# Performance work log

Measured on AMD Instinct MI355X. Metric: run time of the kernel, lower is better.

## Reference

```python
import jax, jax.numpy as jnp
import numpy as np

BS, P, D, C, ND, K, NC, H = 32, 196, 512, 100, 51, 50, 800, 8
LAMBDA, BETA, EPS = 0.5, 5.5, 1e-5


def _ln(x, g, b):
    m = x.mean(-1, keepdims=True)
    v = jnp.mean((x - m) ** 2, axis=-1, keepdims=True)
    return (x - m) / jnp.sqrt(v + EPS) * g + b


def _norm(x):
    return x / jnp.linalg.norm(x, axis=-1, keepdims=True)


def _bonder(x, kv, Wq, Wk, Wv, Wo, ln1_g, ln1_b, ln2_g, ln2_b, W1, b1, W2, b2):
    # cross-attn block: queries = text prompts [B,N,d], kv = retrieved patch feats [B,M,d]
    B, N, d = x.shape
    M = kv.shape[1]
    dh = d // H
    q = (_ln(x, ln1_g, ln1_b) @ Wq).reshape(B, N, H, dh)
    k = (kv @ Wk).reshape(B, M, H, dh)
    v = (kv @ Wv).reshape(B, M, H, dh)
    att = jax.nn.softmax(jnp.einsum('bnhd,bmhd->bhnm', q, k) / np.sqrt(dh).astype(np.float32), axis=-1)
    o = jnp.einsum('bhnm,bmhd->bnhd', att, v).reshape(B, N, d) @ Wo
    x = x + o
    h = _ln(x, ln2_g, ln2_b)
    return x + jax.nn.gelu(h @ W1 + b1) @ W2 + b2


def _dense_logits(gfeat, local, all_text, mean_text, topk):
    # gfeat [b,d], local [b,p,d], all_text [C,n,d], mean_text [C,d]
    base = gfeat @ mean_text.T                                   # [b,C]
    w = jnp.einsum('bd,bpd->bp', gfeat, local)                   # [b,p]
    atf = jnp.transpose(all_text, (1, 0, 2))                     # [n,C,d]
    v = jax.nn.softmax(jnp.einsum('cd,ncd->nc', mean_text, atf), axis=0)  # [n,C]
    sim = jnp.einsum('bpd,ncd->bcpn', local, atf)                # [b,C,p,n]
    vals, idx = jax.lax.top_k(jnp.transpose(sim, (0, 1, 3, 2)), topk)     # over patch dim
    sim_topk = jnp.transpose(vals, (0, 1, 3, 2))                 # [b,C,k,n]
    idx = jnp.transpose(idx, (0, 1, 3, 2))                       # [b,C,k,n]
    idx_w = idx[:, 0, :, 0]                                      # [b,k]
    w_topk = jax.nn.softmax(jnp.take_along_axis(w, idx_w, axis=1), axis=-1)  # [b,k]
    weight = jnp.einsum('bk,nc->bckn', w_topk, v)                # [b,C,k,n]
    return base + jnp.sum(sim_topk * weight, axis=(-2, -1))


def setup_inputs() -> dict:
    key = jax.random.key(0)
    ks = jax.random.split(key, 12)
    s = 0.02
    labels = jax.random.randint(ks[10], (BS,), 0, C)
    cache_labels = jax.random.randint(ks[11], (NC,), 0, C)
    return {
        'local_feat': jax.random.normal(ks[0], (BS, P, D)),
        'Wa': jnp.eye(D) + s * jax.random.normal(ks[1], (D, D)),
        'text_cache': jax.random.normal(ks[2], (C, ND, D)),
        'Wq': s * jax.random.normal(ks[3], (D, D)),
        'Wk': s * jax.random.normal(ks[4], (D, D)),
        'Wv': s * jax.random.normal(ks[5], (D, D)),
        'Wo': s * jax.random.normal(ks[6], (D, D)),
        'ln1_g': jnp.ones((D,)), 'ln1_b': jnp.zeros((D,)),
        'ln2_g': jnp.ones((D,)), 'ln2_b': jnp.zeros((D,)),
        'W1': s * jax.random.normal(ks[7], (D, 4 * D)), 'b1': jnp.zeros((4 * D,)),
        'W2': s * jax.random.normal(ks[8], (4 * D, D)), 'b2': jnp.zeros((D,)),
        'logit_scale': jnp.asarray(np.log(1.0 / 0.07), jnp.float32),
        'ensemble_scale': jnp.asarray(-2.0, jnp.float32),
        'raw_cache_local_feats': jax.random.normal(ks[9], (NC, P, D)),
        'cache_values': jax.nn.one_hot(cache_labels, C, dtype=jnp.float32),
        'labels': labels,
        'cache_labels': cache_labels,
    }


def reference(local_feat, Wa, text_cache, Wq, Wk, Wv, Wo, ln1_g, ln1_b, ln2_g, ln2_b,
              W1, b1, W2, b2, logit_scale, ensemble_scale, raw_cache_local_feats,
              cache_values, labels, cache_labels):
    bs = local_feat.shape[0]
    adapted_local = _norm(local_feat @ Wa.T)                      # [b,p,d]
    adapted_global = _norm(adapted_local.mean(axis=1))            # [b,d]
    base_text_mean = _norm(jax.lax.stop_gradient(text_cache).mean(axis=1))  # [C,d]
    sim_to_text = jax.lax.stop_gradient(adapted_local @ base_text_mean.T)   # [b,p,C]
    sim_target = sim_to_text[jnp.arange(bs), :, labels]           # [b,p]
    topk_idx = jax.lax.top_k(sim_target, K)[1]
    botk_idx = jax.lax.top_k(-sim_target, K)[1]
    topk_feats = jnp.take_along_axis(adapted_local, topk_idx[:, :, None], axis=1)  # [b,K,d]
    botk_feats = jnp.take_along_axis(adapted_local, botk_idx[:, :, None], axis=1)
    # training branch: bonder on ground-truth class prompts, scatter into bias_full
    l2p = text_cache[labels]                                      # [b,ND,d]
    text_bias = _bonder(l2p, jax.lax.stop_gradient(topk_feats),
                        Wq, Wk, Wv, Wo, ln1_g, ln1_b, ln2_g, ln2_b, W1, b1, W2, b2)
    bias_full = jnp.zeros((bs, C, ND, D), local_feat.dtype).at[jnp.arange(bs), labels].set(text_bias)
    bias_avg = bias_full.mean(axis=0)                             # [C,ND,d]
    refined = text_cache + LAMBDA * bias_avg
    refined_norm = _norm(refined)
    refined_mean_norm = _norm(refined_norm.mean(axis=1))
    ls = jnp.exp(logit_scale)
    inter = ls * _dense_logits(adapted_global, adapted_local, refined_norm, refined_mean_norm, K)
    # tip-adapter cache branch
    cache_adapted = _norm(raw_cache_local_feats @ Wa.T)           # [Nc,p,d]
    cache_sim = jax.lax.stop_gradient(cache_adapted @ base_text_mean.T)
    cache_sim_target = cache_sim[jnp.arange(cache_sim.shape[0]), :, cache_labels]
    cache_topk_idx = jax.lax.top_k(cache_sim_target, K)[1]
    cache_topk_feats = jnp.take_along_axis(cache_adapted, cache_topk_idx[:, :, None], axis=1)
    cache_keys = _norm(cache_topk_feats.mean(axis=1))             # [Nc,d]
    query_keys = _norm(topk_feats.mean(axis=1))                   # [b,d]
    affinity = jnp.exp(-BETA * (1.0 - query_keys @ cache_keys.T))
    intra = affinity @ cache_values                               # [b,C]
    scale = jax.nn.sigmoid(ensemble_scale)
    logits = inter * (1 - scale) + intra * ls * scale
    return (logits, inter, intra, adapted_global, topk_feats, botk_feats, refined_norm)
```

## Files before the change

### kernel.cpp

```cpp
#include <hip/hip_runtime.h>
#include <math.h>

#define DEV static __device__ __forceinline__

typedef __attribute__((ext_vector_type(8))) short short8v;
typedef __attribute__((ext_vector_type(8))) _Float16 half8v;
typedef __attribute__((ext_vector_type(4))) float f32x4;

DEV unsigned encf(float f){ unsigned b=__float_as_uint(f); return b ^ (0x80000000u | (unsigned)((int)b>>31)); }
DEV unsigned long long pkvi(float v, int idx){
  return ((unsigned long long)encf(v)<<32) | (unsigned long long)(0xffffffffu - (unsigned)idx);
}
DEV unsigned long long wave_max_ull(unsigned long long u){
  #pragma unroll
  for (int m=1;m<64;m<<=1){ unsigned long long o = __shfl_xor(u, m); if (o>u) u=o; }
  return u;
}
DEV float wave_sum(float v){
  #pragma unroll
  for (int m=32;m;m>>=1) v += __shfl_xor(v, m);
  return v;
}
DEV float blk_sum256(float v, float* scr){
  v = wave_sum(v);
  __syncthreads();
  if ((threadIdx.x & 63)==0) scr[threadIdx.x>>6] = v;
  __syncthreads();
  return scr[0]+scr[1]+scr[2]+scr[3];
}
DEV float gelu_f(float x){ return 0.5f*x*(1.f + tanhf(0.7978845608028654f*(x + 0.044715f*x*x*x))); }
DEV unsigned short f2bf(float x){
  unsigned u = __float_as_uint(x);
  unsigned r = (u + 0x7fffu + ((u>>16)&1u)) >> 16;
  return (unsigned short)r;
}
DEV float bf2f(unsigned short h){ return __uint_as_float(((unsigned)h)<<16); }
DEV void gld16(const void* g, void* l){
  __builtin_amdgcn_global_load_lds((const __attribute__((address_space(1))) unsigned int*)g,
                                   (__attribute__((address_space(3))) unsigned int*)l, 16, 0, 0);
}
template<int CTRL>
DEV float dppf(float x){
  return __int_as_float(__builtin_amdgcn_mov_dpp(__float_as_int(x), CTRL, 0xF, 0xF, false));
}

template<bool TRANSB, int EPI>
__global__ __launch_bounds__(256,2) void gemm128(
  const float* __restrict__ A, const float* __restrict__ B, float* __restrict__ Cp,
  const int M, const int N, const int K,
  const float* __restrict__ bias, const float* __restrict__ resid)
{
  __shared__ float As[16][132];
  __shared__ float Bs[16][132];
  const int t = threadIdx.x;
  const int row0 = blockIdx.x*128, col0 = blockIdx.y*128;
  const int tx = t & 15, ty = t >> 4;
  float acc[8][8];
  #pragma unroll
  for (int i=0;i<8;++i)
    #pragma unroll
    for (int j=0;j<8;++j) acc[i][j]=0.f;

  for (int k0=0; k0<K; k0+=16){
    #pragma unroll
    for (int it=0; it<2; ++it){
      int f = t + it*256;
      int m = f >> 2, kq = (f & 3) << 2;
      float4 v = make_float4(0.f,0.f,0.f,0.f);
      int gr = row0 + m;
      if (gr < M) v = *(const float4*)(A + (size_t)gr*K + (k0+kq));
      As[kq+0][m]=v.x; As[kq+1][m]=v.y; As[kq+2][m]=v.z; As[kq+3][m]=v.w;
    }
    if (TRANSB){
      #pragma unroll
      for (int it=0; it<2; ++it){
        int f = t + it*256;
        int n = f >> 2, kq = (f & 3) << 2;
        float4 v = make_float4(0.f,0.f,0.f,0.f);
        int gc = col0 + n;
        if (gc < N) v = *(const float4*)(B + (size_t)gc*K + (k0+kq));
        Bs[kq+0][n]=v.x; Bs[kq+1][n]=v.y; Bs[kq+2][n]=v.z; Bs[kq+3][n]=v.w;
      }
    } else {
      #pragma unroll
      for (int it=0; it<2; ++it){
        int f = t + it*256;
        int kk = f >> 5, n4 = (f & 31) << 2;
        float4 v = *(const float4*)(B + (size_t)(k0+kk)*N + (col0+n4));
        *(float4*)&Bs[kk][n4] = v;
      }
    }
    __syncthreads();
    #pragma unroll
    for (int k=0;k<16;++k){
      float a[8], bb[8];
      *(float4*)&a[0] = *(const float4*)&As[k][ty*4];
      *(float4*)&a[4] = *(const float4*)&As[k][64+ty*4];
      *(float4*)&bb[0] = *(const float4*)&Bs[k][tx*4];
      *(float4*)&bb[4] = *(const float4*)&Bs[k][64+tx*4];
      #pragma unroll
      for (int i=0;i<8;++i)
        #pragma unroll
        for (int j=0;j<8;++j) acc[i][j] = fmaf(a[i], bb[j], acc[i][j]);
    }
    __syncthreads();
  }

  #pragma unroll
  for (int i=0;i<8;++i){
    int gr = row0 + ((i<4)? (ty*4+i) : (64+ty*4+i-4));
    if (gr >= M) continue;
    #pragma unroll
    for (int jb=0;jb<2;++jb){
      int gc = col0 + (jb? (64+tx*4) : (tx*4));
      float4 vv;
      vv.x = acc[i][jb*4+0]; vv.y = acc[i][jb*4+1]; vv.z = acc[i][jb*4+2]; vv.w = acc[i][jb*4+3];
      if (EPI & 1){
        const float4 bv = *(const float4*)(bias + gc);
        vv.x += bv.x; vv.y += bv.y; vv.z += bv.z; vv.w += bv.w;
      }
      if (EPI & 2){
        vv.x = gelu_f(vv.x); vv.y = gelu_f(vv.y); vv.z = gelu_f(vv.z); vv.w = gelu_f(vv.w);
      }
      if (EPI & 4){
        const float4 rv = *(const float4*)(resid + (size_t)gr*N + gc);
        vv.x += rv.x; vv.y += rv.y; vv.z += rv.z; vv.w += rv.w;
      }
      *(float4*)(Cp + (size_t)gr*N + gc) = vv;
    }
  }
}

template<bool TRANS, bool SUBI>
__global__ __launch_bounds__(256) void k_convw(const float* __restrict__ W,
    unsigned short* __restrict__ hi, unsigned short* __restrict__ lo, int R, int C){
  int n = blockIdx.x;
  int K = TRANS ? R : C;
  for (int k = threadIdx.x; k < K; k += 256){
    float x = TRANS ? W[(size_t)k*C + n] : W[(size_t)n*C + k];
    if (SUBI && k==n) x -= 1.f;
    unsigned short h = f2bf(x);
    hi[(size_t)n*K + k] = h;
    if (lo) lo[(size_t)n*K + k] = f2bf(x - bf2f(h));
  }
}

__global__ __launch_bounds__(256) void k_convw4(
  const float* __restrict__ Wq, const float* __restrict__ Wk,
  const float* __restrict__ Wv, const float* __restrict__ Wo,
  unsigned short* __restrict__ qh, unsigned short* __restrict__ ql,
  unsigned short* __restrict__ kh, unsigned short* __restrict__ kl,
  unsigned short* __restrict__ vh, unsigned short* __restrict__ vl,
  unsigned short* __restrict__ oh, unsigned short* __restrict__ ol)
{
  int n = blockIdx.x;
  const float* W; unsigned short *hi, *lo;
  switch(blockIdx.y){
    case 0: W=Wq; hi=qh; lo=ql; break;
    case 1: W=Wk; hi=kh; lo=kl; break;
    case 2: W=Wv; hi=vh; lo=vl; break;
    default: W=Wo; hi=oh; lo=ol; break;
  }
  for (int k = threadIdx.x; k < 512; k += 256){
    float x = W[(size_t)k*512 + n];
    unsigned short h = f2bf(x);
    hi[(size_t)n*512 + k] = h;
    lo[(size_t)n*512 + k] = f2bf(x - bf2f(h));
  }
}

__global__ __launch_bounds__(256) void k_convd2(const float* __restrict__ Wa, unsigned short* __restrict__ Dfrag){
  int e = blockIdx.x;
  int tile = e>>4, lr = e&15;
  for (int d = threadIdx.x; d < 512; d += 256){
    float x = Wa[(size_t)e*512 + d] - (e==d ? 1.f : 0.f);
    union { _Float16 hh; unsigned short u; } cv;
    cv.hh = (_Float16)x;
    int ks = d>>5, q = (d>>3)&3, el = d&7;
    Dfrag[(size_t)(((tile*16+ks)*64 + q*16 + lr)*8 + el)] = cv.u;
  }
}

template<int EPI>
__global__ __launch_bounds__(256,2) void gemmMF(
  const float* __restrict__ A, const unsigned short* __restrict__ Bhi,
  const unsigned short* __restrict__ Blo, float* __restrict__ Cp,
  const int M, const int N, const int K,
  const float* __restrict__ bias, const float* __restrict__ resid)
{
  __shared__ __align__(16) char sm[32768];
  const int t = threadIdx.x, lane = t&63, wid = t>>6;
  const int row0 = blockIdx.x*128, col0 = blockIdx.y*128;
  f32x4 acc[2][8];
  #pragma unroll
  for (int i=0;i<2;++i)
    #pragma unroll
    for (int j=0;j<8;++j) acc[i][j] = (f32x4){0.f,0.f,0.f,0.f};

  int offA[2], offB[8];
  #pragma unroll
  for (int mt=0; mt<2; ++mt){
    int row = (2*wid+mt)*16 + (lane&15);
    int sp = (lane>>4) ^ ((row>>1)&3);
    offA[mt] = row*64 + sp*16;
  }
  #pragma unroll
  for (int nt=0; nt<8; ++nt){
    int row = nt*16 + (lane&15);
    int sp = (lane>>4) ^ ((row>>1)&3);
    offB[nt] = row*64 + sp*16;
  }

  const int nks = K >> 5;
  for (int ks=0; ks<nks; ++ks){
    #pragma unroll
    for (int i=0;i<2;++i){
      int s = i*256 + t, row = s>>2, sl2 = s&3, phys = sl2 ^ ((row>>1)&3);
      int gr = row0 + row;
      float4 p0 = make_float4(0.f,0.f,0.f,0.f), p1 = p0;
      if (gr < M){
        const float* gp = A + (size_t)gr*K + ks*32 + sl2*8;
        p0 = *(const float4*)gp; p1 = *(const float4*)(gp+4);
      }
      float xs[8] = {p0.x,p0.y,p0.z,p0.w,p1.x,p1.y,p1.z,p1.w};
      union { unsigned short u[8]; float4 f; } uh, ul;
      #pragma unroll
      for (int u=0;u<8;++u){
        unsigned short h = f2bf(xs[u]);
        uh.u[u] = h;
        ul.u[u] = f2bf(xs[u] - bf2f(h));
      }
      *(float4*)(sm + row*64 + phys*16) = uh.f;
      *(float4*)(sm + 8192 + row*64 + phys*16) = ul.f;
    }
    #pragma unroll
    for (int i=0;i<2;++i){
      int s = i*256 + t, row = s>>2, sl2 = s&3, slog = sl2 ^ ((row>>1)&3);
      size_t goff = (size_t)(col0+row)*K + ks*32 + slog*8;
      gld16(Bhi + goff, sm + 16384 + (i*256 + wid*64)*16);
      gld16(Blo + goff, sm + 24576 + (i*256 + wid*64)*16);
    }
    __syncthreads();
    short8v ah0 = *(short8v*)(sm + offA[0]);
    short8v ah1 = *(short8v*)(sm + offA[1]);
    short8v al0 = *(short8v*)(sm + 8192 + offA[0]);
    short8v al1 = *(short8v*)(sm + 8192 + offA[1]);
    #pragma unroll
    for (int nt=0; nt<8; ++nt){
      short8v bh = *(short8v*)(sm + 16384 + offB[nt]);
      short8v bl = *(short8v*)(sm + 24576 + offB[nt]);
      acc[0][nt] = __builtin_amdgcn_mfma_f32_16x16x32_bf16(ah0, bh, acc[0][nt], 0,0,0);
      acc[0][nt] = __builtin_amdgcn_mfma_f32_16x16x32_bf16(ah0, bl, acc[0][nt], 0,0,0);
      acc[0][nt] = __builtin_amdgcn_mfma_f32_16x16x32_bf16(al0, bh, acc[0][nt], 0,0,0);
      acc[1][nt] = __builtin_amdgcn_mfma_f32_16x16x32_bf16(ah1, bh, acc[1][nt], 0,0,0);
      acc[1][nt] = __builtin_amdgcn_mfma_f32_16x16x32_bf16(ah1, bl, acc[1][nt], 0,0,0);
      acc[1][nt] = __builtin_amdgcn_mfma_f32_16x16x32_bf16(al1, bh, acc[1][nt], 0,0,0);
    }
    __syncthreads();
  }

  #pragma unroll
  for (int mt=0; mt<2; ++mt){
    #pragma unroll
    for (int nt=0; nt<8; ++nt){
      int n = col0 + nt*16 + (lane&15);
      int mb = row0 + (2*wid+mt)*16 + (lane>>4)*4;
      #pragma unroll
      for (int j=0;j<4;++j){
        int m = mb + j;
        if (m < M){
          float v = acc[mt][nt][j];
          if (EPI & 1) v += bias[n];
          if (EPI & 2) v = gelu_f(v);
          if (EPI & 4) v += resid[(size_t)m*N + n];
          Cp[(size_t)m*N + n] = v;
        }
      }
    }
  }
}

__global__ __launch_bounds__(512,1) void k_un7(
  const float* __restrict__ raw, const unsigned short* __restrict__ Dfrag,
  const float* __restrict__ zm, const int* __restrict__ clab,
  float* __restrict__ cdot, float* __restrict__ norm2)
{
  __shared__ __align__(16) char Alds[131072];
  __shared__ float n2sq[128];
  __shared__ float n2x[4][128];
  const int t = threadIdx.x, lane = t&63;
  const int wid = t>>6, wm = wid>>2, wn = wid&3;
  const int m0 = blockIdx.x*128;

  {
    const int row = t>>2, sl = t&3;
    const int slg = sl ^ ((row>>1)&3);
    const float* rp = raw + ((size_t)(m0+row))*512 + slg*8;
    const float* zp = zm + (size_t)clab[(m0+row)/196]*512 + slg*8;
    float sq=0.f, cd=0.f;
    for (int ks=0; ks<16; ++ks){
      float4 p0 = *(const float4*)(rp + ks*32);
      float4 p1 = *(const float4*)(rp + ks*32 + 4);
      float4 z0 = *(const float4*)(zp + ks*32);
      float4 z1 = *(const float4*)(zp + ks*32 + 4);
      float xs[8] = {p0.x,p0.y,p0.z,p0.w,p1.x,p1.y,p1.z,p1.w};
      float zs[8] = {z0.x,z0.y,z0.z,z0.w,z1.x,z1.y,z1.z,z1.w};
      union { _Float16 h[8]; f32x4 f; } uh;
      #pragma unroll
      for (int u=0;u<8;++u){
        uh.h[u] = (_Float16)xs[u];
        sq = fmaf(xs[u],xs[u],sq);
        cd = fmaf(xs[u],zs[u],cd);
      }
      *(f32x4*)(Alds + ks*8192 + t*16) = uh.f;
    }
    sq += __shfl_xor(sq,1); sq += __shfl_xor(sq,2);
    cd += __shfl_xor(cd,1); cd += __shfl_xor(cd,2);
    if (sl==0){ n2sq[row] = sq; cdot[m0+row] = cd; }
  }
  __syncthreads();

  int offA[4];
  #pragma unroll
  for (int mt=0; mt<4; ++mt){
    int row = wm*64 + mt*16 + (lane&15);
    int sp = (lane>>4) ^ ((row>>1)&3);
    offA[mt] = row*64 + sp*16;
  }
  const half8v* Dv = (const half8v*)Dfrag;

  float pacc[4][4];
  #pragma unroll
  for (int a_=0;a_<4;++a_)
    #pragma unroll
    for (int b_=0;b_<4;++b_) pacc[a_][b_]=0.f;

  for (int eb2=0; eb2<4; ++eb2){
    f32x4 acc[4][2];
    #pragma unroll
    for (int a_=0;a_<4;++a_)
      #pragma unroll
      for (int b_=0;b_<2;++b_) acc[a_][b_] = (f32x4){0.f,0.f,0.f,0.f};

    #pragma unroll 4
    for (int ks=0; ks<16; ++ks){
      half8v af[4], bf[2];
      #pragma unroll
      for (int mt=0; mt<4; ++mt) af[mt] = *(half8v*)(Alds + ks*8192 + offA[mt]);
      #pragma unroll
      for (int nt=0; nt<2; ++nt) bf[nt] = Dv[(size_t)(((eb2*8 + wn*2 + nt)*16 + ks)*64 + lane)];
      #pragma unroll
      for (int mt=0; mt<4; ++mt)
        #pragma unroll
        for (int nt=0; nt<2; ++nt)
          acc[mt][nt] = __builtin_amdgcn_mfma_f32_16x16x32_f16(af[mt], bf[nt], acc[mt][nt], 0,0,0);
    }

    #pragma unroll
    for (int mt=0; mt<4; ++mt){
      #pragma unroll
      for (int j=0;j<4;++j){
        int row = wm*64 + mt*16 + (lane>>4)*4 + j;
        float p = 0.f;
        #pragma unroll
        for (int nt=0; nt<2; ++nt){
          float U = acc[mt][nt][j];
          int eg = eb2*128 + wn*32 + nt*16 + (lane&15);
          int kse = eg>>5, o = eg&31;
          int sll = (o>>3) ^ ((row>>1)&3);
          float rh = (float)*(const _Float16*)(Alds + kse*8192 + row*64 + sll*16 + (o&7)*2);
          p = fmaf(U, 2.f*rh + U, p);
        }
        p += __shfl_xor(p,1); p += __shfl_xor(p,2); p += __shfl_xor(p,4); p += __shfl_xor(p,8);
        pacc[mt][j] += p;
      }
    }
  }

  __syncthreads();
  if ((lane&15)==0){
    #pragma unroll
    for (int mt=0; mt<4; ++mt)
      #pragma unroll
      for (int j=0;j<4;++j)
        n2x[wn][wm*64 + mt*16 + (lane>>4)*4 + j] = pacc[mt][j];
  }
  __syncthreads();
  if (t < 128)
    norm2[m0+t] = n2sq[t] + n2x[0][t] + n2x[1][t] + n2x[2][t] + n2x[3][t];
}

__global__ __launch_bounds__(256) void k_rownorm(const float* __restrict__ in, float* __restrict__ out,
                                                 unsigned short* __restrict__ bfo, int nrows){
  __shared__ float scr[4];
  int r = blockIdx.x, t = threadIdx.x; (void)nrows;
  const float* p = in + (size_t)r*512;
  float x0 = p[t], x1 = p[t+256];
  float ss = blk_sum256(x0*x0 + x1*x1, scr);
  float inv = 1.f/sqrtf(ss);
  float v0 = x0*inv, v1 = x1*inv;
  out[(size_t)r*512 + t] = v0;
  out[(size_t)r*512 + t + 256] = v1;
  if (bfo){
    size_t br = (size_t)(r/196)*256 + (r%196);
    bfo[br*512 + t]     = f2bf(v0);
    bfo[br*512 + t+256] = f2bf(v1);
  }
}

__global__ __launch_bounds__(256) void k_meanrows_norm(const float* __restrict__ in, int nper,
                                                       float* __restrict__ o1, float* __restrict__ o2){
  __shared__ float scr[4];
  int g = blockIdx.x, t = threadIdx.x;
  float s0=0.f, s1=0.f;
  const float* bp = in + (size_t)g*nper*512;
  for (int r=0;r<nper;++r){ s0 += bp[(size_t)r*512+t]; s1 += bp[(size_t)r*512+t+256]; }
  float ss = blk_sum256(s0*s0+s1*s1, scr);
  float inv = 1.f/sqrtf(ss);
  float v0 = s0*inv, v1 = s1*inv;
  o1[(size_t)g*512+t]=v0; o1[(size_t)g*512+t+256]=v1;
  if (o2){ o2[(size_t)g*512+t]=v0; o2[(size_t)g*512+t+256]=v1; }
}

__global__ __launch_bounds__(256) void k_zmat(const float* __restrict__ btm, const float* __restrict__ Wa, float* __restrict__ z){
  int c = blockIdx.x, t = threadIdx.x;
  float a0=0.f, a1=0.f;
  for (int d=0; d<512; ++d){
    float bv = btm[c*512+d];
    a0 = fmaf(bv, Wa[(size_t)d*512+t], a0);
    a1 = fmaf(bv, Wa[(size_t)d*512+t+256], a1);
  }
  z[c*512+t]=a0; z[c*512+t+256]=a1;
}

__global__ __launch_bounds__(256) void k_dot_bp(const float* __restrict__ AL, const float* __restrict__ vecs,
                                                const int* __restrict__ sel, float* __restrict__ outv, int mode){
  int wid = blockIdx.x*4 + (threadIdx.x>>6);
  int lane = threadIdx.x & 63;
  int b = wid/196;
  int vrow = sel ? sel[b] : (mode ? 0 : b);
  const float* a = AL + (size_t)wid*512 + lane*8;
  const float* v = vecs + (size_t)vrow*512 + lane*8;
  float4 a0 = *(const float4*)a, a1 = *(const float4*)(a+4);
  float4 v0 = *(const float4*)v, v1 = *(const float4*)(v+4);
  float s = a0.x*v0.x + a0.y*v0.y + a0.z*v0.z + a0.w*v0.w
          + a1.x*v1.x + a1.y*v1.y + a1.z*v1.z + a1.w*v1.w;
  s = wave_sum(s);
  if (lane==0) outv[wid] = s;
}

__global__ __launch_bounds__(256) void k_dot2(const float* __restrict__ AL, const float* __restrict__ AGw,
                                              const float* __restrict__ RN00,
                                              float* __restrict__ wbp, float* __restrict__ sLw){
  int wid = blockIdx.x*4 + (threadIdx.x>>6);
  int lane = threadIdx.x & 63;
  int b = wid/196;
  const float* a = AL + (size_t)wid*512 + lane*8;
  const float* v = AGw + (size_t)b*512 + lane*8;
  const float* w = RN00 + lane*8;
  float4 a0=*(const float4*)a, a1=*(const float4*)(a+4);
  float4 v0=*(const float4*)v, v1=*(const float4*)(v+4);
  float4 w0=*(const float4*)w, w1=*(const float4*)(w+4);
  float s1 = a0.x*v0.x+a0.y*v0.y+a0.z*v0.z+a0.w*v0.w + a1.x*v1.x+a1.y*v1.y+a1.z*v1.z+a1.w*v1.w;
  float s2 = a0.x*w0.x+a0.y*w0.y+a0.z*w0.z+a0.w*w0.w + a1.x*w1.x+a1.y*w1.y+a1.z*w1.z+a1.w*w1.w;
  s1 = wave_sum(s1); s2 = wave_sum(s2);
  if (lane==0){ wbp[wid] = s1; sLw[wid] = s2; }
}

__global__ __launch_bounds__(64) void k_topbot(const float* __restrict__ st, int* __restrict__ tki, int* __restrict__ bki){
  int b = blockIdx.x, lane = threadIdx.x;
  float v[4];
  #pragma unroll
  for (int s2=0;s2<4;++s2){ int p = lane + 64*s2; v[s2] = (p<196)? st[b*196+p] : -INFINITY; }
  for (int k=0;k<50;++k){
    unsigned long long best = pkvi(v[0], lane);
    { unsigned long long cc=pkvi(v[1],lane+64);  if(cc>best)best=cc; }
    { unsigned long long cc=pkvi(v[2],lane+128); if(cc>best)best=cc; }
    { unsigned long long cc=pkvi(v[3],lane+192); if(cc>best)best=cc; }
    best = wave_max_ull(best);
    int widx = (int)(0xffffffffu - (unsigned)(best & 0xffffffffu));
    if (lane==0) tki[b*50+k] = widx;
    if ((widx & 63)==lane) v[widx>>6] = -INFINITY;
  }
  #pragma unroll
  for (int s2=0;s2<4;++s2){ int p = lane + 64*s2; v[s2] = (p<196)? -st[b*196+p] : -INFINITY; }
  for (int k=0;k<50;++k){
    unsigned long long best = pkvi(v[0], lane);
    { unsigned long long cc=pkvi(v[1],lane+64);  if(cc>best)best=cc; }
    { unsigned long long cc=pkvi(v[2],lane+128); if(cc>best)best=cc; }
    { unsigned long long cc=pkvi(v[3],lane+192); if(cc>best)best=cc; }
    best = wave_max_ull(best);
    int widx = (int)(0xffffffffu - (unsigned)(best & 0xffffffffu));
    if (lane==0) bki[b*50+k] = widx;
    if ((widx & 63)==lane) v[widx>>6] = -INFINITY;
  }
}

__global__ __launch_bounds__(256) void k_gather_tb(const float* __restrict__ AL, const int* __restrict__ tki, const int* __restrict__ bki,
                                                   float* __restrict__ otk, float* __restrict__ obk, float* __restrict__ qk){
  __shared__ float scr[4];
  int b = blockIdx.x, t = threadIdx.x;
  float a0=0.f, a1=0.f;
  for (int k=0;k<50;++k){
    int pt = tki[b*50+k];
    const float* rp = AL + ((size_t)b*196+pt)*512;
    float x0 = rp[t], x1 = rp[t+256];
    otk[((size_t)b*50+k)*512 + t] = x0; otk[((size_t)b*50+k)*512 + t+256] = x1;
    a0 += x0; a1 += x1;
    int pb = bki[b*50+k];
    const float* rb = AL + ((size_t)b*196+pb)*512;
    obk[((size_t)b*50+k)*512 + t] = rb[t]; obk[((size_t)b*50+k)*512 + t+256] = rb[t+256];
  }
  float ss = blk_sum256(a0*a0+a1*a1, scr);
  float inv = 1.f/sqrtf(ss);
  qk[b*512+t] = a0*inv; qk[b*512+t+256] = a1*inv;
}

__global__ __launch_bounds__(256) void k_gather_x(const float* __restrict__ tc, const int* __restrict__ labels, float* __restrict__ xb){
  int r = blockIdx.x, t = threadIdx.x;
  int b = r/51, n = r%51;
  int lab = labels[b];
  const float* src = tc + ((size_t)lab*51 + n)*512;
  xb[(size_t)r*512+t] = src[t]; xb[(size_t)r*512+t+256] = src[t+256];
}

__global__ __launch_bounds__(256) void k_layernorm(const float* __restrict__ in, float* __restrict__ out,
                                                   const float* __restrict__ g, const float* __restrict__ be){
  __shared__ float scr[4];
  int r = blockIdx.x, t = threadIdx.x;
  const float* p = in + (size_t)r*512;
  float x0=p[t], x1=p[t+256];
  float s = blk_sum256(x0+x1, scr);
  float mean = s*(1.f/512.f);
  float ss = blk_sum256(x0*x0+x1*x1, scr);
  float var = ss*(1.f/512.f) - mean*mean;
  float inv = 1.f/sqrtf(var + 1e-5f);
  out[(size_t)r*512+t]     = (x0-mean)*inv*g[t]     + be[t];
  out[(size_t)r*512+t+256] = (x1-mean)*inv*g[t+256] + be[t+256];
}

__global__ __launch_bounds__(256) void k_attn(const float* __restrict__ qb, const float* __restrict__ kb,
                                              const float* __restrict__ vb, float* __restrict__ ob){
  int b = blockIdx.x, h = blockIdx.y, t = threadIdx.x;
  __shared__ float qh[51][65];
  __shared__ float kh[50][65];
  __shared__ float vh[50][65];
  __shared__ float S[51][52];
  for (int f=t; f<51*64; f+=256){ int n=f>>6, d=f&63; qh[n][d] = qb[((size_t)(b*51+n))*512 + h*64 + d]; }
  for (int f=t; f<50*64; f+=256){ int m=f>>6, d=f&63;
    kh[m][d] = kb[((size_t)(b*50+m))*512 + h*64 + d];
    vh[m][d] = vb[((size_t)(b*50+m))*512 + h*64 + d];
  }
  __syncthreads();
  for (int f=t; f<51*50; f+=256){
    int n=f/50, m=f%50;
    float s=0.f;
    #pragma unroll 8
    for (int d=0; d<64; ++d) s = fmaf(qh[n][d], kh[m][d], s);
    S[n][m] = s*0.125f;
  }
  __syncthreads();
  int w = t>>6, lane = t&63;
  for (int n=w; n<51; n+=4){
    float x = (lane<50)? S[n][lane] : -INFINITY;
    float mx = x;
    #pragma unroll
    for (int m2=32;m2;m2>>=1) mx = fmaxf(mx, __shfl_xor(mx,m2));
    float e = (lane<50)? expf(x-mx) : 0.f;
    float se = wave_sum(e);
    if (lane<50) S[n][lane] = e/se;
  }
  __syncthreads();
  for (int f=t; f<51*64; f+=256){
    int n=f>>6, d=f&63;
    float s=0.f;
    #pragma unroll 10
    for (int m=0;m<50;++m) s = fmaf(S[n][m], vh[m][d], s);
    ob[((size_t)(b*51+n))*512 + h*64 + d] = s;
  }
}

__global__ __launch_bounds__(256) void k_refined(const float* __restrict__ tc, const float* __restrict__ TB,
                                                 const int* __restrict__ labels, float* __restrict__ RN,
                                                 unsigned short* __restrict__ RNbf){
  __shared__ float scr[4];
  __shared__ int labL[32];
  int blk = blockIdx.x, t = threadIdx.x;
  int c = blk/51, n = blk%51;
  if (t<32) labL[t] = labels[t];
  __syncthreads();
  float r0=0.f, r1=0.f;
  for (int b=0;b<32;++b){
    if (labL[b]==c){
      const float* tb = TB + ((size_t)(b*51+n))*512;
      r0 += tb[t]; r1 += tb[t+256];
    }
  }
  const float* tcp = tc + ((size_t)(c*51+n))*512;
  r0 = tcp[t]     + r0*(1.f/64.f);
  r1 = tcp[t+256] + r1*(1.f/64.f);
  float ss = blk_sum256(r0*r0+r1*r1, scr);
  float inv = 1.f/sqrtf(ss);
  float v0 = r0*inv, v1 = r1*inv;
  RN[((size_t)(c*51+n))*512+t]     = v0;
  RN[((size_t)(c*51+n))*512+t+256] = v1;
  size_t br = (size_t)c*64 + n;
  RNbf[br*512 + t]     = f2bf(v0);
  RNbf[br*512 + t+256] = f2bf(v1);
}

__global__ __launch_bounds__(256) void k_vsm(const float* __restrict__ RN, const float* __restrict__ RMN, float* __restrict__ vsm){
  __shared__ float sv[51];
  int c = blockIdx.x, t = threadIdx.x, w = t>>6, lane = t&63;
  for (int n=w; n<51; n+=4){
    const float* a = RN + ((size_t)(c*51+n))*512 + lane*8;
    const float* m = RMN + (size_t)c*512 + lane*8;
    float4 a0=*(const float4*)a, a1=*(const float4*)(a+4);
    float4 m0=*(const float4*)m, m1=*(const float4*)(m+4);
    float s = a0.x*m0.x+a0.y*m0.y+a0.z*m0.z+a0.w*m0.w + a1.x*m1.x+a1.y*m1.y+a1.z*m1.z+a1.w*m1.w;
    s = wave_sum(s);
    if (lane==0) sv[n]=s;
  }
  __syncthreads();
  if (t<64){
    float x = (t<51)? sv[t] : -INFINITY;
    float mx = x;
    #pragma unroll
    for (int m2=32;m2;m2>>=1) mx = fmaxf(mx, __shfl_xor(mx,m2));
    float e = (t<51)? expf(x-mx) : 0.f;
    float se = wave_sum(e);
    if (t<51) vsm[c*51+t] = e/se;
  }
}

__global__ __launch_bounds__(64) void k_wtopk(const float* __restrict__ sLg,
                                              const float* __restrict__ wbp, float* __restrict__ wtk){
  __shared__ int idxL[50];
  int b = blockIdx.x, lane = threadIdx.x;
  float v[4];
  #pragma unroll
  for (int s2=0;s2<4;++s2){ int p = lane+64*s2; v[s2] = (p<196)? sLg[b*196+p] : -INFINITY; }
  for (int k=0;k<50;++k){
    unsigned long long best = pkvi(v[0], lane);
    { unsigned long long cc=pkvi(v[1],lane+64);  if(cc>best)best=cc; }
    { unsigned long long cc=pkvi(v[2],lane+128); if(cc>best)best=cc; }
    { unsigned long long cc=pkvi(v[3],lane+192); if(cc>best)best=cc; }
    best = wave_max_ull(best);
    int widx = (int)(0xffffffffu - (unsigned)(best & 0xffffffffu));
    if (lane==0) idxL[k]=widx;
    if ((widx&63)==lane) v[widx>>6] = -INFINITY;
  }
  __syncthreads();
  float wv = (lane<50)? wbp[b*196 + idxL[lane]] : -INFINITY;
  float mx = wv;
  #pragma unroll
  for (int m2=32;m2;m2>>=1) mx = fmaxf(mx, __shfl_xor(mx,m2));
  float e = (lane<50)? expf(wv-mx) : 0.f;
  float se = wave_sum(e);
  if (lane<50) wtk[b*50+lane] = e/se;
}

__global__ __launch_bounds__(256,3) void k_dense3(
  const unsigned short* __restrict__ ALbf, const unsigned short* __restrict__ RNbf,
  const float* __restrict__ RMN, const float* __restrict__ AG,
  const float* __restrict__ vsm, const float* __restrict__ wtk,
  const float* __restrict__ lsp, float* __restrict__ interw)
{
  __shared__ __align__(16) char smem[52224];
  __shared__ float red[8];
  __shared__ float wtkS[52];
  const int c = blockIdx.x, b = blockIdx.y;
  const int t = threadIdx.x, lane = t&63, wid = t>>6;

  if (t<50) wtkS[t] = wtk[b*50+t];
  if (t<64){
    const float* a = AG + (size_t)b*512 + t*8;
    const float* m = RMN + (size_t)c*512 + t*8;
    float4 a0=*(const float4*)a, a1=*(const float4*)(a+4);
    float4 m0=*(const float4*)m, m1=*(const float4*)(m+4);
    float s = a0.x*m0.x+a0.y*m0.y+a0.z*m0.z+a0.w*m0.w + a1.x*m1.x+a1.y*m1.y+a1.z*m1.z+a1.w*m1.w;
    s = wave_sum(s);
    if (t==0) red[4] = s;
  }

  f32x4 acc[4][4];
  #pragma unroll
  for (int i=0;i<4;++i)
    #pragma unroll
    for (int j=0;j<4;++j) acc[i][j] = (f32x4){0.f,0.f,0.f,0.f};

  int offA[4], offB[4];
  #pragma unroll
  for (int mt=0; mt<4; ++mt){
    int row = wid*64 + mt*16 + (lane&15);
    int sp = (lane>>4) ^ ((row>>1)&3);
    offA[mt] = row*64 + sp*16;
  }
  #pragma unroll
  for (int nt=0; nt<4; ++nt){
    int row = nt*16 + (lane&15);
    int sp = (lane>>4) ^ ((row>>1)&3);
    offB[nt] = row*64 + sp*16;
  }

  const unsigned short* Abase = ALbf + ((size_t)b<<17);
  const unsigned short* Bbase = RNbf + ((size_t)c<<15);

  auto STAGE = [&](int buf, int ks){
    const int Ab = buf? 20480 : 0, Bb = buf? 36864 : 16384;
    #pragma unroll
    for (int i=0;i<4;++i){
      int q = i*256 + t;
      int row = q>>2, sl = q&3;
      int slog = sl ^ ((row>>1)&3);
      gld16(Abase + ((size_t)row<<9) + ks*32 + slog*8, smem + Ab + (i*256 + wid*64)*16);
    }
    {
      int row = t>>2, sl = t&3;
      int slog = sl ^ ((row>>1)&3);
      gld16(Bbase + ((size_t)row<<9) + ks*32 + slog*8, smem + Bb + (wid*64)*16);
    }
  };

  STAGE(0, 0);
  __syncthreads();
  for (int ks=0; ks<16; ++ks){
    const int cur = ks&1;
    if (ks<15) STAGE(cur^1, ks+1);
    const int Ab = cur? 20480 : 0, Bb = cur? 36864 : 16384;
    short8v af[4], bf[4];
    #pragma unroll
    for (int mt=0; mt<4; ++mt) af[mt] = *(short8v*)(smem + Ab + offA[mt]);
    #pragma unroll
    for (int nt=0; nt<4; ++nt) bf[nt] = *(short8v*)(smem + Bb + offB[nt]);
    #pragma unroll
    for (int mt=0; mt<4; ++mt)
      #pragma unroll
      for (int nt=0; nt<4; ++nt)
        acc[mt][nt] = __builtin_amdgcn_mfma_f32_16x16x32_bf16(af[mt], bf[nt], acc[mt][nt], 0,0,0);
    __syncthreads();
  }

  #pragma unroll
  for (int mt=0; mt<4; ++mt){
    #pragma unroll
    for (int nt=0; nt<4; ++nt){
      int n = nt*16 + (lane&15);
      if (n < 51){
        int p0 = wid*64 + mt*16 + (lane>>4)*4;
        int addr = ((n<<10) + (p0<<2)) ^ ((((n&7)^wid)&7)<<4);
        *(f32x4*)(smem + addr) = acc[mt][nt];
      }
    }
  }
  __syncthreads();

  const int n = wid*16 + (lane>>2);
  const int q = lane&3;
  float v[64];
  if (n < 51){
    #pragma unroll
    for (int i=0;i<16;++i){
      int p = q*64 + i*4;
      int addr = ((n<<10) + (p<<2)) ^ ((((n&7)^q)&7)<<4);
      *(f32x4*)&v[i*4] = *(f32x4*)(smem + addr);
    }
  } else {
    #pragma unroll
    for (int i=0;i<64;++i) v[i] = -INFINITY;
  }
  if (q==3){
    #pragma unroll
    for (int j=4;j<64;++j) v[j] = -INFINITY;
  }

  #pragma unroll
  for (int k=2;k<=64;k<<=1){
    #pragma unroll
    for (int j=k>>1;j>=1;j>>=1){
      #pragma unroll
      for (int i=0;i<64;++i){
        if ((i&j)==0){
          int p2 = i|j;
          float a=v[i], bb=v[p2];
          if ((i&k)!=0){ v[i]=fminf(a,bb); v[p2]=fmaxf(a,bb); }
          else         { v[i]=fmaxf(a,bb); v[p2]=fminf(a,bb); }
        }
      }
    }
  }
  #pragma unroll
  for (int i=0;i<32;++i){
    float pa = dppf<0xB1>(v[63-i]);
    float pb = dppf<0xB1>(v[i]);
    v[i]    = fmaxf(v[i], pa);
    v[63-i] = fmaxf(v[63-i], pb);
  }
  #pragma unroll
  for (int j=32;j>=1;j>>=1){
    #pragma unroll
    for (int i=0;i<64;++i){
      if ((i&j)==0){ int p2=i|j; float a=v[i],bb=v[p2]; v[i]=fmaxf(a,bb); v[p2]=fminf(a,bb); }
    }
  }
  #pragma unroll
  for (int i=0;i<32;++i){
    float pa = dppf<0x4E>(v[63-i]);
    float pb = dppf<0x4E>(v[i]);
    v[i]    = fmaxf(v[i], pa);
    v[63-i] = fmaxf(v[63-i], pb);
  }
  #pragma unroll
  for (int j=32;j>=1;j>>=1){
    #pragma unroll
    for (int i=0;i<64;++i){
      if ((i&j)==0){ int p2=i|j; float a=v[i],bb=v[p2]; v[i]=fmaxf(a,bb); v[p2]=fminf(a,bb); }
    }
  }

  float s = 0.f;
  #pragma unroll
  for (int r=0;r<50;++r) s = fmaf(wtkS[r], v[r], s);
  float val = (q==0 && n<51) ? vsm[c*51+n]*s : 0.f;
  val = wave_sum(val);
  if (lane==0) red[wid] = val;
  __syncthreads();
  if (t==0){
    float ls = expf(lsp[0]);
    interw[b*100+c] = ls*(red[4] + red[0]+red[1]+red[2]+red[3]);
  }
}

__global__ __launch_bounds__(256) void k_cache_sel(const float* __restrict__ cdot, const float* __restrict__ norm2,
                                                   const float* __restrict__ raw, float* __restrict__ rbar){
  __shared__ int idxL[50];
  __shared__ float invL[50];
  int i = blockIdx.x, t = threadIdx.x;
  if (t < 64){
    int lane = t;
    float v[4];
    #pragma unroll
    for (int s2=0;s2<4;++s2){
      int p = lane+64*s2;
      v[s2] = (p<196)? cdot[(size_t)i*196+p] * (1.f/sqrtf(norm2[(size_t)i*196+p])) : -INFINITY;
    }
    for (int k=0;k<50;++k){
      unsigned long long best = pkvi(v[0], lane);
      { unsigned long long cc=pkvi(v[1],lane+64);  if(cc>best)best=cc; }
      { unsigned long long cc=pkvi(v[2],lane+128); if(cc>best)best=cc; }
      { unsigned long long cc=pkvi(v[3],lane+192); if(cc>best)best=cc; }
      best = wave_max_ull(best);
      int widx = (int)(0xffffffffu - (unsigned)(best & 0xffffffffu));
      if (lane==0){ idxL[k]=widx; invL[k] = 1.f/sqrtf(norm2[(size_t)i*196+widx]); }
      if ((widx&63)==lane) v[widx>>6] = -INFINITY;
    }
  }
  __syncthreads();
  float a0=0.f, a1=0.f;
  for (int k=0;k<50;++k){
    int p = idxL[k]; float iv = invL[k];
    const float* rp = raw + ((size_t)i*196+p)*512;
    a0 = fmaf(rp[t], iv, a0);
    a1 = fmaf(rp[t+256], iv, a1);
  }
  rbar[(size_t)i*512+t]=a0; rbar[(size_t)i*512+t+256]=a1;
}

__global__ __launch_bounds__(256) void k_aff(const float* __restrict__ qk, const float* __restrict__ ck, float* __restrict__ aff){
  int gid = blockIdx.x*4 + (threadIdx.x>>6);
  int lane = threadIdx.x&63;
  int b = gid/800, i = gid%800;
  const float* a = qk + (size_t)b*512 + lane*8;
  const float* v = ck + (size_t)i*512 + lane*8;
  float4 a0=*(const float4*)a, a1=*(const float4*)(a+4);
  float4 v0=*(const float4*)v, v1=*(const float4*)(v+4);
  float s = a0.x*v0.x+a0.y*v0.y+a0.z*v0.z+a0.w*v0.w + a1.x*v1.x+a1.y*v1.y+a1.z*v1.z+a1.w*v1.w;
  s = wave_sum(s);
  if (lane==0) aff[gid] = expf(-5.5f*(1.f - s));
}

__global__ __launch_bounds__(128) void k_intra(const float* __restrict__ aff, const float* __restrict__ cv, float* __restrict__ intra){
  __shared__ float affL[800];
  int b = blockIdx.x, t = threadIdx.x;
  for (int f=t; f<800; f+=128) affL[f] = aff[b*800+f];
  __syncthreads();
  if (t<100){
    float s=0.f;
    for (int i=0;i<800;++i) s = fmaf(affL[i], cv[(size_t)i*100+t], s);
    intra[b*100+t]=s;
  }
}

__global__ void k_final(const float* __restrict__ interw, const float* __restrict__ intraw,
                        const float* __restrict__ lsp, const float* __restrict__ esp, float* __restrict__ outp){
  int idx = blockIdx.x*256 + threadIdx.x;
  if (idx < 3200){
    float ls = expf(lsp[0]);
    float sc = 1.f/(1.f + expf(-esp[0]));
    float iv = interw[idx], ia = intraw[idx];
    outp[idx]        = iv*(1.f-sc) + ia*ls*sc;
    outp[3200+idx]   = iv;
    outp[6400+idx]   = ia;
  }
}

extern "C" void kernel_launch(void* const* d_in, const int* in_sizes, int n_in,
                              void* d_out, int out_size, void* d_ws, size_t ws_size,
                              hipStream_t stream)
{
  (void)in_sizes; (void)n_in; (void)out_size; (void)ws_size;
  const float* lf   = (const float*)d_in[0];
  const float* Wa   = (const float*)d_in[1];
  const float* tc   = (const float*)d_in[2];
  const float* Wq   = (const float*)d_in[3];
  const float* Wk   = (const float*)d_in[4];
  const float* Wv   = (const float*)d_in[5];
  const float* Wo   = (const float*)d_in[6];
  const float* ln1g = (const float*)d_in[7];
  const float* ln1b = (const float*)d_in[8];
  const float* ln2g = (const float*)d_in[9];
  const float* ln2b = (const float*)d_in[10];
  const float* W1   = (const float*)d_in[11];
  const float* b1   = (const float*)d_in[12];
  const float* W2   = (const float*)d_in[13];
  const float* b2   = (const float*)d_in[14];
  const float* lsp  = (const float*)d_in[15];
  const float* esp  = (const float*)d_in[16];
  const float* raw  = (const float*)d_in[17];
  const float* cv   = (const float*)d_in[18];
  const int* labels = (const int*)d_in[19];
  const int* clab   = (const int*)d_in[20];

  float* out = (float*)d_out;
  float* outAG = out + 9600;
  float* outTK = out + 25984;
  float* outBK = out + 845184;
  float* outRN = out + 1664384;

  float* wsf = (float*)d_ws;
  size_t o = 0;
  #define WALLOC(name, n) float* name = wsf + o; o += (size_t)(n);
  WALLOC(AL,    6272*512)
  WALLOC(xb,    1632*512)
  WALLOC(ln1x,  1632*512)
  WALLOC(qb,    1632*512)
  WALLOC(kb,    1600*512)
  WALLOC(vbuf,  1600*512)
  WALLOC(ob,    1632*512)
  WALLOC(x2,    1632*512)
  WALLOC(h2,    1632*512)
  WALLOC(y1g,   (size_t)1632*2048)
  WALLOC(TB,    1632*512)
  WALLOC(btm,   100*512)
  WALLOC(zm,    100*512)
  WALLOC(RMN,   100*512)
  WALLOC(vsm,   5100)
  WALLOC(st,    6272)
  WALLOC(wbp,   6272)
  WALLOC(sLw,   6272)
  WALLOC(AGw,   32*512)
  WALLOC(qkb,   32*512)
  WALLOC(wtk,   1600)
  WALLOC(norm2, 156800)
  WALLOC(cdot,  156800)
  WALLOC(rbar,  800*512)
  WALLOC(mbuf,  800*512)
  WALLOC(ckb,   800*512)
  WALLOC(aff,   25600)
  WALLOC(interw,3200)
  WALLOC(intraw,3200)
  #undef WALLOC
  int* tki = (int*)(wsf + o); o += 1600;
  int* bki = (int*)(wsf + o); o += 1600;
  unsigned short* ALbf = (unsigned short*)(wsf + o); o += (size_t)32*256*512/2;
  unsigned short* RNbf = (unsigned short*)(wsf + o); o += (size_t)100*64*512/2;
  #define WALLOC16(name, n) unsigned short* name = (unsigned short*)(wsf + o); o += ((size_t)(n))/2;
  WALLOC16(waHi, 262144)  WALLOC16(waLo, 262144)
  WALLOC16(wqHi, 262144)  WALLOC16(wqLo, 262144)
  WALLOC16(wkHi, 262144)  WALLOC16(wkLo, 262144)
  WALLOC16(wvHi, 262144)  WALLOC16(wvLo, 262144)
  WALLOC16(woHi, 262144)  WALLOC16(woLo, 262144)
  WALLOC16(w1Hi, 1048576) WALLOC16(w1Lo, 1048576)
  WALLOC16(w2Hi, 1048576) WALLOC16(w2Lo, 1048576)
  WALLOC16(dfrag, 262144)
  #undef WALLOC16

  k_convw<false,false><<<dim3(512), dim3(256), 0, stream>>>(Wa, waHi, waLo, 512,512);
  k_convw4<<<dim3(512,4), dim3(256), 0, stream>>>(Wq,Wk,Wv,Wo, wqHi,wqLo, wkHi,wkLo, wvHi,wvLo, woHi,woLo);
  k_convw<true ,false><<<dim3(2048), dim3(256), 0, stream>>>(W1, w1Hi, w1Lo, 512,2048);
  k_convw<true ,false><<<dim3(512), dim3(256), 0, stream>>>(W2, w2Hi, w2Lo, 2048,512);
  k_convd2<<<dim3(512), dim3(256), 0, stream>>>(Wa, dfrag);

  hipMemsetAsync(ALbf, 0, (size_t)32*256*512*2, stream);
  hipMemsetAsync(RNbf, 0, (size_t)100*64*512*2, stream);

  gemm128<true,0><<<dim3(49,4), dim3(256), 0, stream>>>(lf, Wa, AL, 6272,512,512, nullptr,nullptr);
  k_rownorm<<<dim3(6272), dim3(256), 0, stream>>>(AL, AL, ALbf, 6272);
  k_meanrows_norm<<<dim3(32), dim3(256), 0, stream>>>(AL, 196, AGw, outAG);
  k_meanrows_norm<<<dim3(100), dim3(256), 0, stream>>>(tc, 51, btm, (float*)nullptr);
  k_zmat<<<dim3(100), dim3(256), 0, stream>>>(btm, Wa, zm);
  k_dot_bp<<<dim3(1568), dim3(256), 0, stream>>>(AL, btm, labels, st, 0);
  k_topbot<<<dim3(32), dim3(64), 0, stream>>>(st, tki, bki);
  k_gather_tb<<<dim3(32), dim3(256), 0, stream>>>(AL, tki, bki, outTK, outBK, qkb);
  k_gather_x<<<dim3(1632), dim3(256), 0, stream>>>(tc, labels, xb);
  k_layernorm<<<dim3(1632), dim3(256), 0, stream>>>(xb, ln1x, ln1g, ln1b);
  gemmMF<0><<<dim3(13,4), dim3(256), 0, stream>>>(ln1x, wqHi, wqLo, qb, 1632,512,512, nullptr,nullptr);
  gemmMF<0><<<dim3(13,4), dim3(256), 0, stream>>>(outTK, wkHi, wkLo, kb, 1600,512,512, nullptr,nullptr);
  gemmMF<0><<<dim3(13,4), dim3(256), 0, stream>>>(outTK, wvHi, wvLo, vbuf, 1600,512,512, nullptr,nullptr);
  k_attn<<<dim3(32,8), dim3(256), 0, stream>>>(qb, kb, vbuf, ob);
  gemmMF<4><<<dim3(13,4), dim3(256), 0, stream>>>(ob, woHi, woLo, x2, 1632,512,512, nullptr, xb);
  k_layernorm<<<dim3(1632), dim3(256), 0, stream>>>(x2, h2, ln2g, ln2b);
  gemmMF<3><<<dim3(13,16), dim3(256), 0, stream>>>(h2, w1Hi, w1Lo, y1g, 1632,2048,512, b1, nullptr);
  gemmMF<5><<<dim3(13,4), dim3(256), 0, stream>>>(y1g, w2Hi, w2Lo, TB, 1632,512,2048, b2, x2);
  k_refined<<<dim3(5100), dim3(256), 0, stream>>>(tc, TB, labels, outRN, RNbf);
  k_meanrows_norm<<<dim3(100), dim3(256), 0, stream>>>(outRN, 51, RMN, (float*)nullptr);
  k_vsm<<<dim3(100), dim3(256), 0, stream>>>(outRN, RMN, vsm);
  k_dot2<<<dim3(1568), dim3(256), 0, stream>>>(AL, AGw, outRN, wbp, sLw);
  k_wtopk<<<dim3(32), dim3(64), 0, stream>>>(sLw, wbp, wtk);
  k_dense3<<<dim3(100,32), dim3(256), 0, stream>>>(ALbf, RNbf, RMN, AGw, vsm, wtk, lsp, interw);
  k_un7<<<dim3(1225), dim3(512), 0, stream>>>(raw, dfrag, zm, clab, cdot, norm2);
  k_cache_sel<<<dim3(800), dim3(256), 0, stream>>>(cdot, norm2, raw, rbar);
  gemmMF<0><<<dim3(7,4), dim3(256), 0, stream>>>(rbar, waHi, waLo, mbuf, 800,512,512, nullptr,nullptr);
  k_rownorm<<<dim3(800), dim3(256), 0, stream>>>(mbuf, ckb, (unsigned short*)nullptr, 800);
  k_aff<<<dim3(6400), dim3(256), 0, stream>>>(qkb, ckb, aff);
  k_intra<<<dim3(32), dim3(128), 0, stream>>>(aff, cv, intraw);
  k_final<<<dim3(13), dim3(256), 0, stream>>>(interw, intraw, lsp, esp, out);
}
```

Before: 1.167 ms.

## Halve cache-norm kernel tile to 64 rows for two blocks per CU

```diff
diff --git a/kernel.cpp b/kernel.cpp
--- a/kernel.cpp
+++ b/kernel.cpp
@@ -280,25 +280,28 @@
   }
 }
 
-__global__ __launch_bounds__(512,1) void k_un7(
+__global__ __launch_bounds__(512,2) void k_un8(
   const float* __restrict__ raw, const unsigned short* __restrict__ Dfrag,
   const float* __restrict__ zm, const int* __restrict__ clab,
   float* __restrict__ cdot, float* __restrict__ norm2)
 {
-  __shared__ __align__(16) char Alds[131072];
-  __shared__ float n2sq[128];
-  __shared__ float n2x[4][128];
+  __shared__ __align__(16) char Alds[65536];
+  __shared__ float n2sq[64];
+  __shared__ float n2x[4][64];
   const int t = threadIdx.x, lane = t&63;
-  const int wid = t>>6, wm = wid>>2, wn = wid&3;
-  const int m0 = blockIdx.x*128;
+  const int wid = t>>6, wm = wid&1, wn = wid>>1;
+  const int m0 = blockIdx.x*64;
 
   {
-    const int row = t>>2, sl = t&3;
+    const int row = t>>3, rem = t&7;
+    const int sl = rem&3, ksh = rem>>2;
     const int slg = sl ^ ((row>>1)&3);
     const float* rp = raw + ((size_t)(m0+row))*512 + slg*8;
     const float* zp = zm + (size_t)clab[(m0+row)/196]*512 + slg*8;
     float sq=0.f, cd=0.f;
-    for (int ks=0; ks<16; ++ks){
+    #pragma unroll
+    for (int i=0;i<8;++i){
+      int ks = i*2 + ksh;
       float4 p0 = *(const float4*)(rp + ks*32);
       float4 p1 = *(const float4*)(rp + ks*32 + 4);
       float4 z0 = *(const float4*)(zp + ks*32);
@@ -312,81 +315,63 @@
         sq = fmaf(xs[u],xs[u],sq);
         cd = fmaf(xs[u],zs[u],cd);
       }
-      *(f32x4*)(Alds + ks*8192 + t*16) = uh.f;
-    }
-    sq += __shfl_xor(sq,1); sq += __shfl_xor(sq,2);
-    cd += __shfl_xor(cd,1); cd += __shfl_xor(cd,2);
-    if (sl==0){ n2sq[row] = sq; cdot[m0+row] = cd; }
-  }
-  __syncthreads();
-
-  int offA[4];
-  #pragma unroll
-  for (int mt=0; mt<4; ++mt){
-    int row = wm*64 + mt*16 + (lane&15);
+      *(f32x4*)(Alds + ks*4096 + row*64 + sl*16) = uh.f;
+    }
+    sq += __shfl_xor(sq,1); sq += __shfl_xor(sq,2); sq += __shfl_xor(sq,4);
+    cd += __shfl_xor(cd,1); cd += __shfl_xor(cd,2); cd += __shfl_xor(cd,4);
+    if (rem==0){ n2sq[row] = sq; cdot[m0+row] = cd; }
+  }
+  __syncthreads();
+
+  int offA[2];
+  #pragma unroll
+  for (int mt=0; mt<2; ++mt){
+    int row = wm*32 + mt*16 + (lane&15);
     int sp = (lane>>4) ^ ((row>>1)&3);
     offA[mt] = row*64 + sp*16;
   }
   const half8v* Dv = (const half8v*)Dfrag;
 
-  float pacc[4][4];
-  #pragma unroll
-  for (int a_=0;a_<4;++a_)
-    #pragma unroll
-    for (int b_=0;b_<4;++b_) pacc[a_][b_]=0.f;
-
-  for (int eb2=0; eb2<4; ++eb2){
-    f32x4 acc[4][2];
-    #pragma unroll
-    for (int a_=0;a_<4;++a_)
+  f32x4 acc[2][8];
+  #pragma unroll
+  for (int a_=0;a_<2;++a_)
+    #pragma unroll
+    for (int b_=0;b_<8;++b_) acc[a_][b_] = (f32x4){0.f,0.f,0.f,0.f};
+
+  #pragma unroll 2
+  for (int ks=0; ks<16; ++ks){
+    half8v af[2];
+    #pragma unroll
+    for (int mt=0; mt<2; ++mt) af[mt] = *(half8v*)(Alds + ks*4096 + offA[mt]);
+    #pragma unroll
+    for (int nt=0; nt<8; ++nt){
+      half8v bf = Dv[(size_t)(((wn*8 + nt)*16 + ks)*64 + lane)];
+      acc[0][nt] = __builtin_amdgcn_mfma_f32_16x16x32_f16(af[0], bf, acc[0][nt], 0,0,0);
+      acc[1][nt] = __builtin_amdgcn_mfma_f32_16x16x32_f16(af[1], bf, acc[1][nt], 0,0,0);
+    }
+  }
+
+  #pragma unroll
+  for (int mt=0; mt<2; ++mt){
+    #pragma unroll
+    for (int j=0;j<4;++j){
+      int row = wm*32 + mt*16 + (lane>>4)*4 + j;
+      float p = 0.f;
       #pragma unroll
-      for (int b_=0;b_<2;++b_) acc[a_][b_] = (f32x4){0.f,0.f,0.f,0.f};
-
-    #pragma unroll 4
-    for (int ks=0; ks<16; ++ks){
-      half8v af[4], bf[2];
-      #pragma unroll
-      for (int mt=0; mt<4; ++mt) af[mt] = *(half8v*)(Alds + ks*8192 + offA[mt]);
-      #pragma unroll
-      for (int nt=0; nt<2; ++nt) bf[nt] = Dv[(size_t)(((eb2*8 + wn*2 + nt)*16 + ks)*64 + lane)];
-      #pragma unroll
-      for (int mt=0; mt<4; ++mt)
-        #pragma unroll
-        for (int nt=0; nt<2; ++nt)
-          acc[mt][nt] = __builtin_amdgcn_mfma_f32_16x16x32_f16(af[mt], bf[nt], acc[mt][nt], 0,0,0);
-    }
-
-    #pragma unroll
-    for (int mt=0; mt<4; ++mt){
-      #pragma unroll
-      for (int j=0;j<4;++j){
-        int row = wm*64 + mt*16 + (lane>>4)*4 + j;
-        float p = 0.f;
-        #pragma unroll
-        for (int nt=0; nt<2; ++nt){
-          float U = acc[mt][nt][j];
-          int eg = eb2*128 + wn*32 + nt*16 + (lane&15);
-          int kse = eg>>5, o = eg&31;
-          int sll = (o>>3) ^ ((row>>1)&3);
-          float rh = (float)*(const _Float16*)(Alds + kse*8192 + row*64 + sll*16 + (o&7)*2);
-          p = fmaf(U, 2.f*rh + U, p);
-        }
-        p += __shfl_xor(p,1); p += __shfl_xor(p,2); p += __shfl_xor(p,4); p += __shfl_xor(p,8);
-        pacc[mt][j] += p;
-      }
-    }
-  }
-
-  __syncthreads();
-  if ((lane&15)==0){
-    #pragma unroll
-    for (int mt=0; mt<4; ++mt)
-      #pragma unroll
-      for (int j=0;j<4;++j)
-        n2x[wn][wm*64 + mt*16 + (lane>>4)*4 + j] = pacc[mt][j];
-  }
-  __syncthreads();
-  if (t < 128)
+      for (int nt=0; nt<8; ++nt){
+        float U = acc[mt][nt][j];
+        int eg = wn*128 + nt*16 + (lane&15);
+        int kse = eg>>5, o = eg&31;
+        int sll = (o>>3) ^ ((row>>1)&3);
+        float rh = (float)*(const _Float16*)(Alds + kse*4096 + row*64 + sll*16 + (o&7)*2);
+        p = fmaf(U, 2.f*rh + U, p);
+      }
+      p += __shfl_xor(p,1); p += __shfl_xor(p,2); p += __shfl_xor(p,4); p += __shfl_xor(p,8);
+      if ((lane&15)==0) n2x[wn][row] = p;
+    }
+  }
+  __syncthreads();
+  if (t < 64)
     norm2[m0+t] = n2sq[t] + n2x[0][t] + n2x[1][t] + n2x[2][t] + n2x[3][t];
 }
 
@@ -1018,7 +1003,7 @@
   k_dot2<<<dim3(1568), dim3(256), 0, stream>>>(AL, AGw, outRN, wbp, sLw);
   k_wtopk<<<dim3(32), dim3(64), 0, stream>>>(sLw, wbp, wtk);
   k_dense3<<<dim3(100,32), dim3(256), 0, stream>>>(ALbf, RNbf, RMN, AGw, vsm, wtk, lsp, interw);
-  k_un7<<<dim3(1225), dim3(512), 0, stream>>>(raw, dfrag, zm, clab, cdot, norm2);
+  k_un8<<<dim3(2450), dim3(512), 0, stream>>>(raw, dfrag, zm, clab, cdot, norm2);
   k_cache_sel<<<dim3(800), dim3(256), 0, stream>>>(cdot, norm2, raw, rbar);
   gemmMF<0><<<dim3(7,4), dim3(256), 0, stream>>>(rbar, waHi, waLo, mbuf, 800,512,512, nullptr,nullptr);
   k_rownorm<<<dim3(800), dim3(256), 0, stream>>>(mbuf, ckb, (unsigned short*)nullptr, 800);
```

Result: slower. 1.228 ms (+5.3%).
